# Performance work log

Hardware: AMD Instinct MI355X
Metric: run time of the kernel (lower is better)

The kernel has to match this reference:

```python
import jax, jax.numpy as jnp
from jax import lax
import numpy as np

BN_EPS = 1e-3  # ultralytics BatchNorm2d default eps

def setup_inputs() -> dict:
    key = jax.random.key(0)
    ks = jax.random.split(key, 6)
    B, C, H, W = 16, 64, 160, 160
    E, R = 4, 16  # experts, reduced router dim = C // reduction
    return {
        "x": jax.random.normal(ks[0], (B, C, H, W), jnp.float32),
        "fc1_w": jax.random.normal(ks[1], (R, C), jnp.float32) * 0.1,
        "fc2_w": jax.random.normal(ks[2], (E, R), jnp.float32) * 0.1,
        "fc2_b": jax.random.normal(ks[3], (E,), jnp.float32) * 0.1,
        "conv_w": jax.random.normal(ks[4], (E, C, C, 3, 3), jnp.float32) * 0.05,
        "bn_gamma": jnp.ones((E, C), jnp.float32),
        "bn_beta": jnp.zeros((E, C), jnp.float32),
        "bn_mean": jax.random.normal(ks[5], (E, C), jnp.float32) * 0.1,
        "bn_var": jnp.ones((E, C), jnp.float32),
    }

def reference(x, fc1_w, fc2_w, fc2_b, conv_w, bn_gamma, bn_beta, bn_mean, bn_var):
    # Router: global avg pool -> fc1 -> relu -> fc2 -> softmax over experts
    g = jnp.mean(x, axis=(2, 3))                       # [B, C]
    h = jax.nn.relu(g @ fc1_w.T)                       # [B, R]
    w = jax.nn.softmax(h @ fc2_w.T + fc2_b, axis=1)    # [B, E]

    def expert(kernel, gamma, beta, mean, var):
        # Conv2d(bias=False, pad=k//2) + BatchNorm2d (eval) + SiLU
        y = lax.conv_general_dilated(
            x, kernel, window_strides=(1, 1), padding="SAME",
            dimension_numbers=("NCHW", "OIHW", "NCHW"))
        scale = (gamma * lax.rsqrt(var + BN_EPS))[None, :, None, None]
        shift = (beta - mean * gamma * lax.rsqrt(var + BN_EPS))[None, :, None, None]
        return jax.nn.silu(y * scale + shift)          # [B, Co, H, W]

    outs = jax.vmap(expert)(conv_w, bn_gamma, bn_beta, bn_mean, bn_var)  # [E, B, Co, H, W]
    return jnp.einsum("ebchw,be->bchw", outs, w)
```

## Files before the change

kernel.cpp:

```cpp
#include <hip/hip_runtime.h>
#include <hip/hip_bf16.h>

typedef unsigned short u16;
typedef unsigned int   u32;
typedef __attribute__((ext_vector_type(8))) short s16x8;
typedef __attribute__((ext_vector_type(16))) float f32x16;

#define BN_EPS 1e-3f
#define NB 16
#define NC 64
#define NH 160
#define NW 160
#define HP 162
#define WPD 162

#define OFF_XT 0UL
#define SZ_XT  (16UL*162*162*64*2)
#define OFF_WT (OFF_XT + SZ_XT)
#define SZ_WT  (4UL*64*9*64*2)
#define OFF_SH (OFF_WT + SZ_WT)
#define OFF_G  (OFF_SH + 1024UL)
#define OFF_WE (OFF_G + 4096UL)
#define OFF_GP (OFF_WE + 256UL)

#define XSTRIDE 342
#define XLS_BYTES (8 * XSTRIDE * 16)
#define WLS_BYTES (2304 * 16)
#define SHLS_BYTES 1024
#define SMEM_TOTAL (XLS_BYTES + WLS_BYTES + SHLS_BYTES)

__device__ __forceinline__ u16 f2bf(float f) {
    u32 u = __builtin_bit_cast(u32, f);
    u += 0x7fffu + ((u >> 16) & 1u);
    return (u16)(u >> 16);
}

__global__ void prep_w(const float* __restrict__ cw, u16* __restrict__ wt,
                       const float* __restrict__ gamma, const float* __restrict__ beta,
                       const float* __restrict__ mean, const float* __restrict__ var,
                       float* __restrict__ shift) {
    int idx = blockIdx.x * 256 + threadIdx.x;
    if (idx < 4 * 2 * 9 * 4 * 64 * 8) {
        int cin = idx & 7;
        int t = idx >> 3;
        int co = t & 63; t >>= 6;
        int cio = t & 3; t >>= 2;
        int pos = t % 9; t /= 9;
        int ch = t & 1;
        int e = t >> 1;
        int tsp = (pos % 3) * 3 + (pos / 3);
        int ci = ch * 32 + cio * 8 + cin;
        int ec = e * 64 + co;
        float sc = gamma[ec] * rsqrtf(var[ec] + BN_EPS);
        wt[idx] = f2bf(cw[(((long)ec) * 64 + ci) * 9 + tsp] * sc);
    }
    if (idx < 256) {
        float sc = gamma[idx] * rsqrtf(var[idx] + BN_EPS);
        shift[idx] = beta[idx] - mean[idx] * sc;
    }
}

__global__ void prep_x(const float* __restrict__ x, u16* __restrict__ xt,
                       float* __restrict__ gpart) {
    __shared__ float tile[64][33];
    int blk = blockIdx.x;
    int t = threadIdx.x;
    if (blk >= 12800) {
        int bb = blk - 12800;
        int hp = bb % 162, b = bb / 162;
        u32* row = (u32*)xt + (((long)b * 162 + hp) * 162) * 32;
        if (hp == 0 || hp == 161) {
            for (int i = t; i < 162 * 32; i += 256) row[i] = 0u;
        } else if (t < 64) {
            int p = (t >> 5) ? 161 : 0;
            row[p * 32 + (t & 31)] = 0u;
        }
        return;
    }
    int wt5 = blk % 5;
    int tmp = blk / 5;
    int h = tmp % 160, b = tmp / 160;
    int w0 = wt5 * 32;
    int w = t & 31, c0 = t >> 5;
#pragma unroll
    for (int i = 0; i < 8; ++i) {
        int c = c0 + 8 * i;
        tile[c][w] = x[(((long)b * 64 + c) * 160 + h) * 160 + w0 + w];
    }
    __syncthreads();
    if (t < 64) {
        float s = 0.f;
#pragma unroll
        for (int wi = 0; wi < 32; ++wi) s += tile[t][wi];
        gpart[((long)(b * 64 + t)) * 800 + h * 5 + wt5] = s;
    }
    u32* xt32 = (u32*)xt;
    long base = ((((long)b * 162 + h + 1) * 162) + (w0 + 1)) * 32;
#pragma unroll
    for (int j = 0; j < 4; ++j) {
        int idx = t + 256 * j;
        int p = idx >> 5, cp = idx & 31;
        float v0 = tile[2 * cp][p], v1 = tile[2 * cp + 1][p];
        xt32[base + p * 32 + cp] = (u32)f2bf(v0) | ((u32)f2bf(v1) << 16);
    }
}

__global__ void g_reduce(const float* __restrict__ gpart, float* __restrict__ g) {
    int id = blockIdx.x;
    int t = threadIdx.x;
    float s = 0.f;
    for (int i = t; i < 800; i += 256) s += gpart[(long)id * 800 + i];
#pragma unroll
    for (int off = 32; off > 0; off >>= 1) s += __shfl_down(s, off, 64);
    __shared__ float red[4];
    if ((t & 63) == 0) red[t >> 6] = s;
    __syncthreads();
    if (t == 0) g[id] = (red[0] + red[1] + red[2] + red[3]) * (1.f / 25600.f);
}

__global__ void router(const float* __restrict__ g, const float* __restrict__ fc1w,
                       const float* __restrict__ fc2w, const float* __restrict__ fc2b,
                       float* __restrict__ wexp) {
    __shared__ float gL[16][64];
    __shared__ float h1[16][16];
    __shared__ float z[16][4];
    int t = threadIdx.x;
    for (int i = t; i < 1024; i += 256) gL[i >> 6][i & 63] = g[i];
    __syncthreads();
    {
        int b = t >> 4, r = t & 15;
        float s = 0.f;
#pragma unroll
        for (int c = 0; c < 64; ++c) s += gL[b][c] * fc1w[r * 64 + c];
        h1[b][r] = fmaxf(s, 0.f);
    }
    __syncthreads();
    if (t < 64) {
        int b = t >> 2, e = t & 3;
        float s = fc2b[e];
#pragma unroll
        for (int r = 0; r < 16; ++r) s += h1[b][r] * fc2w[e * 16 + r];
        z[b][e] = s;
    }
    __syncthreads();
    if (t < 16) {
        int b = t;
        float m = fmaxf(fmaxf(z[b][0], z[b][1]), fmaxf(z[b][2], z[b][3]));
        float e0 = __expf(z[b][0] - m), e1 = __expf(z[b][1] - m);
        float e2 = __expf(z[b][2] - m), e3 = __expf(z[b][3] - m);
        float inv = 1.f / (e0 + e1 + e2 + e3);
        wexp[b * 4 + 0] = e0 * inv; wexp[b * 4 + 1] = e1 * inv;
        wexp[b * 4 + 2] = e2 * inv; wexp[b * 4 + 3] = e3 * inv;
    }
}

__global__ __launch_bounds__(256, 2) void conv_main(
    const u16* __restrict__ xt, const u16* __restrict__ wt,
    const float* __restrict__ shift,
    const float* __restrict__ wexp, float* __restrict__ out) {
    extern __shared__ char smem[];
    u16* xls = (u16*)smem;
    u16* wls = (u16*)(smem + XLS_BYTES);
    float* shls = (float*)(smem + XLS_BYTES + WLS_BYTES);

    const int o = blockIdx.x;
    const int blk = (o & 7) * 200 + (o >> 3);
    const int wt5 = blk % 5;
    const int tmp = blk / 5;
    const int ht = tmp % 20;
    const int b = tmp / 20;
    const int h0 = ht * 8, w0 = wt5 * 32;
    const int tid = threadIdx.x;
    const int lane = tid & 63;
    const int wv = tid >> 6;
    const int l31 = lane & 31, kh = lane >> 5;
    const int r0 = 2 * wv;

    {
#pragma unroll
        for (int r = 0; r < 9; ++r) {
            int oo = r * 256 + tid;
            __builtin_amdgcn_global_load_lds(
                (const __attribute__((address_space(1))) void*)(wt + oo * 8),
                (__attribute__((address_space(3))) void*)(wls + oo * 8),
                16, 0, 0);
        }
    }
    const float we0 = wexp[(b << 2) + 0];
    const float we1 = wexp[(b << 2) + 1];
    const float we2 = wexp[(b << 2) + 2];
    const float we3 = wexp[(b << 2) + 3];
    shls[tid] = shift[tid];
    {
        const u16* xb = xt + (long)b * HP * WPD * 64;
        for (int c = tid; c < 2720; c += 256) {
            int P = c >> 3, cg = c & 7;
            int y = P / 34, px = P - y * 34;
            const u16* src = xb + (((long)(h0 + y) * WPD) + (w0 + px)) * 64 + cg * 8;
            s16x8 v = *(const s16x8*)src;
            *(s16x8*)(&xls[(cg * XSTRIDE + P) << 3]) = v;
        }
    }

    const int oA2 = (kh * 64 + l31) << 3;
    const int oBk0 = ((kh * XSTRIDE) + r0 * 34 + l31) << 3;
    const int oBk1 = oBk0 + ((2 * XSTRIDE) << 3);

    f32x16 acc00 = (f32x16)(0.f), acc01 = (f32x16)(0.f);
    f32x16 acc10 = (f32x16)(0.f), acc11 = (f32x16)(0.f);
    f32x16 oac00 = (f32x16)(0.f), oac01 = (f32x16)(0.f);
    f32x16 oac10 = (f32x16)(0.f), oac11 = (f32x16)(0.f);

    auto epi = [&](int E) {
        const float we = (E == 0) ? we0 : (E == 1) ? we1 : (E == 2) ? we2 : we3;
        const float* shE = shls + (E << 6);
#pragma unroll
        for (int j = 0; j < 16; ++j) {
            const int cob = (j & 3) + 8 * (j >> 2) + 4 * kh;
            {
                float sh = shE[cob];
                float y0 = acc00[j] + sh;
                float y1 = acc01[j] + sh;
                oac00[j] += we * (y0 * __builtin_amdgcn_rcpf(1.f + __expf(-y0)));
                oac01[j] += we * (y1 * __builtin_amdgcn_rcpf(1.f + __expf(-y1)));
            }
            {
                float sh = shE[cob + 32];
                float y0 = acc10[j] + sh;
                float y1 = acc11[j] + sh;
                oac10[j] += we * (y0 * __builtin_amdgcn_rcpf(1.f + __expf(-y0)));
                oac11[j] += we * (y1 * __builtin_amdgcn_rcpf(1.f + __expf(-y1)));
            }
        }
        acc00 = (f32x16)(0.f); acc01 = (f32x16)(0.f);
        acc10 = (f32x16)(0.f); acc11 = (f32x16)(0.f);
    };

#pragma unroll 1
    for (int s = 0; s < 8; ++s) {
        const int ch = s & 1;
        const int chU = (ch * 4 * XSTRIDE) << 3;
        const int b0U = oBk0 + chU;
        const int b1U = oBk1 + chU;

        auto dx_group = [&](int g, int pos0) {
            const int gU = g << 3;
            s16x8 B00 = *(const s16x8*)(&xls[b0U + gU]);
            s16x8 B01 = *(const s16x8*)(&xls[b1U + gU]);
            s16x8 B10 = *(const s16x8*)(&xls[b0U + gU + (34 << 3)]);
            s16x8 B11 = *(const s16x8*)(&xls[b1U + gU + (34 << 3)]);
            s16x8 B20 = *(const s16x8*)(&xls[b0U + gU + (68 << 3)]);
            s16x8 B21 = *(const s16x8*)(&xls[b1U + gU + (68 << 3)]);
            s16x8 B30 = *(const s16x8*)(&xls[b0U + gU + (102 << 3)]);
            s16x8 B31 = *(const s16x8*)(&xls[b1U + gU + (102 << 3)]);
            __builtin_amdgcn_s_setprio(1);
#pragma unroll
            for (int dy = 0; dy < 3; ++dy) {
                const int atU = oA2 + (pos0 + dy) * 2048;
                s16x8 a00 = *(const s16x8*)(&wls[atU]);
                s16x8 a10 = *(const s16x8*)(&wls[atU + 256]);
                s16x8 a01 = *(const s16x8*)(&wls[atU + 1024]);
                s16x8 a11 = *(const s16x8*)(&wls[atU + 1280]);
                s16x8 bn00 = (dy == 0) ? B00 : (dy == 1) ? B10 : B20;
                s16x8 bn01 = (dy == 0) ? B01 : (dy == 1) ? B11 : B21;
                s16x8 bn10 = (dy == 0) ? B10 : (dy == 1) ? B20 : B30;
                s16x8 bn11 = (dy == 0) ? B11 : (dy == 1) ? B21 : B31;
                acc00 = __builtin_amdgcn_mfma_f32_32x32x16_bf16(a00, bn00, acc00, 0, 0, 0);
                acc10 = __builtin_amdgcn_mfma_f32_32x32x16_bf16(a10, bn00, acc10, 0, 0, 0);
                acc01 = __builtin_amdgcn_mfma_f32_32x32x16_bf16(a00, bn10, acc01, 0, 0, 0);
                acc11 = __builtin_amdgcn_mfma_f32_32x32x16_bf16(a10, bn10, acc11, 0, 0, 0);
                acc00 = __builtin_amdgcn_mfma_f32_32x32x16_bf16(a01, bn01, acc00, 0, 0, 0);
                acc10 = __builtin_amdgcn_mfma_f32_32x32x16_bf16(a11, bn01, acc10, 0, 0, 0);
                acc01 = __builtin_amdgcn_mfma_f32_32x32x16_bf16(a01, bn11, acc01, 0, 0, 0);
                acc11 = __builtin_amdgcn_mfma_f32_32x32x16_bf16(a11, bn11, acc11, 0, 0, 0);
            }
            __builtin_amdgcn_s_setprio(0);
        };

        if (s == 0) __builtin_amdgcn_s_waitcnt(0x070);
        else        __builtin_amdgcn_s_waitcnt(0xF73);
        __builtin_amdgcn_s_barrier();
        __builtin_amdgcn_sched_barrier(0);
        dx_group(0, 0);
        dx_group(1, 3);

        __builtin_amdgcn_s_waitcnt(0xF70);
        __builtin_amdgcn_s_barrier();
        __builtin_amdgcn_sched_barrier(0);
        if (s < 7) {
            const u16* wsrc = wt + ((long)(s + 1)) * 2304 * 8;
#pragma unroll
            for (int r = 0; r < 6; ++r) {
                int oo = r * 256 + tid;
                __builtin_amdgcn_global_load_lds(
                    (const __attribute__((address_space(1))) void*)(wsrc + oo * 8),
                    (__attribute__((address_space(3))) void*)(wls + oo * 8),
                    16, 0, 0);
            }
        }
        dx_group(2, 6);
        if (ch == 1) epi(s >> 1);

        __builtin_amdgcn_s_barrier();
        __builtin_amdgcn_sched_barrier(0);
        if (s < 7) {
            const u16* wsrc = wt + ((long)(s + 1)) * 2304 * 8;
#pragma unroll
            for (int r = 6; r < 9; ++r) {
                int oo = r * 256 + tid;
                __builtin_amdgcn_global_load_lds(
                    (const __attribute__((address_space(1))) void*)(wsrc + oo * 8),
                    (__attribute__((address_space(3))) void*)(wls + oo * 8),
                    16, 0, 0);
            }
        }
    }

    const int yy = h0 + r0;
#pragma unroll
    for (int j = 0; j < 16; ++j) {
        const int cob = (j & 3) + 8 * (j >> 2) + 4 * kh;
        out[(((long)(b * 64 + cob)) * 160 + yy) * 160 + w0 + l31] = oac00[j];
        out[(((long)(b * 64 + cob)) * 160 + yy + 1) * 160 + w0 + l31] = oac01[j];
        out[(((long)(b * 64 + cob + 32)) * 160 + yy) * 160 + w0 + l31] = oac10[j];
        out[(((long)(b * 64 + cob + 32)) * 160 + yy + 1) * 160 + w0 + l31] = oac11[j];
    }
}

extern "C" void kernel_launch(void* const* d_in, const int* in_sizes, int n_in,
                              void* d_out, int out_size, void* d_ws, size_t ws_size,
                              hipStream_t stream) {
    const float* x = (const float*)d_in[0];
    const float* fc1w = (const float*)d_in[1];
    const float* fc2w = (const float*)d_in[2];
    const float* fc2b = (const float*)d_in[3];
    const float* convw = (const float*)d_in[4];
    const float* gamma = (const float*)d_in[5];
    const float* beta = (const float*)d_in[6];
    const float* mean = (const float*)d_in[7];
    const float* var = (const float*)d_in[8];
    float* out = (float*)d_out;
    char* ws = (char*)d_ws;
    u16* xt = (u16*)(ws + OFF_XT);
    u16* wtb = (u16*)(ws + OFF_WT);
    float* shift = (float*)(ws + OFF_SH);
    float* g = (float*)(ws + OFF_G);
    float* wexp = (float*)(ws + OFF_WE);
    float* gpart = (float*)(ws + OFF_GP);

    hipFuncSetAttribute((const void*)conv_main,
                        hipFuncAttributeMaxDynamicSharedMemorySize, SMEM_TOTAL);

    prep_w<<<576, 256, 0, stream>>>(convw, wtb, gamma, beta, mean, var, shift);
    prep_x<<<15392, 256, 0, stream>>>(x, xt, gpart);
    g_reduce<<<1024, 256, 0, stream>>>(gpart, g);
    router<<<1, 256, 0, stream>>>(g, fc1w, fc2w, fc2b, wexp);
    conv_main<<<1600, 256, SMEM_TOTAL, stream>>>(xt, wtb, shift, wexp, out);
}
```

Measured before the change: 178.4 us.

## Make conv kernel persistent with per-XCD atomic tile queues

Replaces the 1600-block launch with 512 persistent blocks that take tiles from eight per-XCD atomic counters, stealing from other queues when their own runs out. Weight prefetch now wraps around so the next tile's first expert chunk is already loading, which removes per-block launch and ramp-up cost and the tail imbalance. The cost is an extra memset, an atomic and a barrier per tile, and the x-tile load is no longer overlapped with block startup. There is also a possible hazard from the x LDS overwrite racing with the previous tile's reads.

```diff
diff --git a/kernel.cpp b/kernel.cpp
--- a/kernel.cpp
+++ b/kernel.cpp
@@ -21,13 +21,14 @@
 #define OFF_SH (OFF_WT + SZ_WT)
 #define OFF_G  (OFF_SH + 1024UL)
 #define OFF_WE (OFF_G + 4096UL)
-#define OFF_GP (OFF_WE + 256UL)
+#define OFF_CT (OFF_WE + 256UL)
+#define OFF_GP (OFF_CT + 256UL)
 
 #define XSTRIDE 342
 #define XLS_BYTES (8 * XSTRIDE * 16)
 #define WLS_BYTES (2304 * 16)
 #define SHLS_BYTES 1024
-#define SMEM_TOTAL (XLS_BYTES + WLS_BYTES + SHLS_BYTES)
+#define SMEM_TOTAL (XLS_BYTES + WLS_BYTES + SHLS_BYTES + 16)
 
 __device__ __forceinline__ u16 f2bf(float f) {
     u32 u = __builtin_bit_cast(u32, f);
@@ -157,24 +158,20 @@
 __global__ __launch_bounds__(256, 2) void conv_main(
     const u16* __restrict__ xt, const u16* __restrict__ wt,
     const float* __restrict__ shift,
-    const float* __restrict__ wexp, float* __restrict__ out) {
+    const float* __restrict__ wexp, float* __restrict__ out,
+    u32* __restrict__ ctrs) {
     extern __shared__ char smem[];
     u16* xls = (u16*)smem;
     u16* wls = (u16*)(smem + XLS_BYTES);
     float* shls = (float*)(smem + XLS_BYTES + WLS_BYTES);
-
-    const int o = blockIdx.x;
-    const int blk = (o & 7) * 200 + (o >> 3);
-    const int wt5 = blk % 5;
-    const int tmp = blk / 5;
-    const int ht = tmp % 20;
-    const int b = tmp / 20;
-    const int h0 = ht * 8, w0 = wt5 * 32;
+    int* stl = (int*)(smem + XLS_BYTES + WLS_BYTES + SHLS_BYTES);
+
     const int tid = threadIdx.x;
     const int lane = tid & 63;
     const int wv = tid >> 6;
     const int l31 = lane & 31, kh = lane >> 5;
     const int r0 = 2 * wv;
+    const int xb8 = blockIdx.x & 7;
 
     {
 #pragma unroll
@@ -186,145 +183,170 @@
                 16, 0, 0);
         }
     }
-    const float we0 = wexp[(b << 2) + 0];
-    const float we1 = wexp[(b << 2) + 1];
-    const float we2 = wexp[(b << 2) + 2];
-    const float we3 = wexp[(b << 2) + 3];
     shls[tid] = shift[tid];
-    {
-        const u16* xb = xt + (long)b * HP * WPD * 64;
-        for (int c = tid; c < 2720; c += 256) {
-            int P = c >> 3, cg = c & 7;
-            int y = P / 34, px = P - y * 34;
-            const u16* src = xb + (((long)(h0 + y) * WPD) + (w0 + px)) * 64 + cg * 8;
-            s16x8 v = *(const s16x8*)src;
-            *(s16x8*)(&xls[(cg * XSTRIDE + P) << 3]) = v;
-        }
-    }
 
     const int oA2 = (kh * 64 + l31) << 3;
     const int oBk0 = ((kh * XSTRIDE) + r0 * 34 + l31) << 3;
     const int oBk1 = oBk0 + ((2 * XSTRIDE) << 3);
 
-    f32x16 acc00 = (f32x16)(0.f), acc01 = (f32x16)(0.f);
-    f32x16 acc10 = (f32x16)(0.f), acc11 = (f32x16)(0.f);
-    f32x16 oac00 = (f32x16)(0.f), oac01 = (f32x16)(0.f);
-    f32x16 oac10 = (f32x16)(0.f), oac11 = (f32x16)(0.f);
-
-    auto epi = [&](int E) {
-        const float we = (E == 0) ? we0 : (E == 1) ? we1 : (E == 2) ? we2 : we3;
-        const float* shE = shls + (E << 6);
+    for (;;) {
+        if (tid == 0) {
+            int got = -1;
+            for (int d = 0; d < 8; ++d) {
+                int xx = (xb8 + d) & 7;
+                u32 tl = atomicAdd(&ctrs[xx], 1u);
+                if (tl < 200u) { got = xx * 200 + (int)tl; break; }
+            }
+            *stl = got;
+        }
+        __syncthreads();
+        const int blk = *stl;
+        if (blk < 0) break;
+
+        const int wt5 = blk % 5;
+        const int tmp = blk / 5;
+        const int ht = tmp % 20;
+        const int b = tmp / 20;
+        const int h0 = ht * 8, w0 = wt5 * 32;
+
+        const float we0 = wexp[(b << 2) + 0];
+        const float we1 = wexp[(b << 2) + 1];
+        const float we2 = wexp[(b << 2) + 2];
+        const float we3 = wexp[(b << 2) + 3];
+
+        {
+            const u16* xb = xt + (long)b * HP * WPD * 64;
+            for (int c = tid; c < 2720; c += 256) {
+                int P = c >> 3, cg = c & 7;
+                int y = P / 34, px = P - y * 34;
+                const u16* src = xb + (((long)(h0 + y) * WPD) + (w0 + px)) * 64 + cg * 8;
+                s16x8 v = *(const s16x8*)src;
+                *(s16x8*)(&xls[(cg * XSTRIDE + P) << 3]) = v;
+            }
+        }
+
+        f32x16 acc00 = (f32x16)(0.f), acc01 = (f32x16)(0.f);
+        f32x16 acc10 = (f32x16)(0.f), acc11 = (f32x16)(0.f);
+        f32x16 oac00 = (f32x16)(0.f), oac01 = (f32x16)(0.f);
+        f32x16 oac10 = (f32x16)(0.f), oac11 = (f32x16)(0.f);
+
+        auto epi = [&](int E) {
+            const float we = (E == 0) ? we0 : (E == 1) ? we1 : (E == 2) ? we2 : we3;
+            const float* shE = shls + (E << 6);
+#pragma unroll
+            for (int j = 0; j < 16; ++j) {
+                const int cob = (j & 3) + 8 * (j >> 2) + 4 * kh;
+                {
+                    float sh = shE[cob];
+                    float y0 = acc00[j] + sh;
+                    float y1 = acc01[j] + sh;
+                    oac00[j] += we * (y0 * __builtin_amdgcn_rcpf(1.f + __expf(-y0)));
+                    oac01[j] += we * (y1 * __builtin_amdgcn_rcpf(1.f + __expf(-y1)));
+                }
+                {
+                    float sh = shE[cob + 32];
+                    float y0 = acc10[j] + sh;
+                    float y1 = acc11[j] + sh;
+                    oac10[j] += we * (y0 * __builtin_amdgcn_rcpf(1.f + __expf(-y0)));
+                    oac11[j] += we * (y1 * __builtin_amdgcn_rcpf(1.f + __expf(-y1)));
+                }
+            }
+            acc00 = (f32x16)(0.f); acc01 = (f32x16)(0.f);
+            acc10 = (f32x16)(0.f); acc11 = (f32x16)(0.f);
+        };
+
+#pragma unroll 1
+        for (int s = 0; s < 8; ++s) {
+            const int ch = s & 1;
+            const int chU = (ch * 4 * XSTRIDE) << 3;
+            const int b0U = oBk0 + chU;
+            const int b1U = oBk1 + chU;
+            const int sn = (s + 1) & 7;
+
+            auto dx_group = [&](int g, int pos0) {
+                const int gU = g << 3;
+                s16x8 B00 = *(const s16x8*)(&xls[b0U + gU]);
+                s16x8 B01 = *(const s16x8*)(&xls[b1U + gU]);
+                s16x8 B10 = *(const s16x8*)(&xls[b0U + gU + (34 << 3)]);
+                s16x8 B11 = *(const s16x8*)(&xls[b1U + gU + (34 << 3)]);
+                s16x8 B20 = *(const s16x8*)(&xls[b0U + gU + (68 << 3)]);
+                s16x8 B21 = *(const s16x8*)(&xls[b1U + gU + (68 << 3)]);
+                s16x8 B30 = *(const s16x8*)(&xls[b0U + gU + (102 << 3)]);
+                s16x8 B31 = *(const s16x8*)(&xls[b1U + gU + (102 << 3)]);
+                __builtin_amdgcn_s_setprio(1);
+#pragma unroll
+                for (int dy = 0; dy < 3; ++dy) {
+                    const int atU = oA2 + (pos0 + dy) * 2048;
+                    s16x8 a00 = *(const s16x8*)(&wls[atU]);
+                    s16x8 a10 = *(const s16x8*)(&wls[atU + 256]);
+                    s16x8 a01 = *(const s16x8*)(&wls[atU + 1024]);
+                    s16x8 a11 = *(const s16x8*)(&wls[atU + 1280]);
+                    s16x8 bn00 = (dy == 0) ? B00 : (dy == 1) ? B10 : B20;
+                    s16x8 bn01 = (dy == 0) ? B01 : (dy == 1) ? B11 : B21;
+                    s16x8 bn10 = (dy == 0) ? B10 : (dy == 1) ? B20 : B30;
+                    s16x8 bn11 = (dy == 0) ? B11 : (dy == 1) ? B21 : B31;
+                    acc00 = __builtin_amdgcn_mfma_f32_32x32x16_bf16(a00, bn00, acc00, 0, 0, 0);
+                    acc10 = __builtin_amdgcn_mfma_f32_32x32x16_bf16(a10, bn00, acc10, 0, 0, 0);
+                    acc01 = __builtin_amdgcn_mfma_f32_32x32x16_bf16(a00, bn10, acc01, 0, 0, 0);
+                    acc11 = __builtin_amdgcn_mfma_f32_32x32x16_bf16(a10, bn10, acc11, 0, 0, 0);
+                    acc00 = __builtin_amdgcn_mfma_f32_32x32x16_bf16(a01, bn01, acc00, 0, 0, 0);
+                    acc10 = __builtin_amdgcn_mfma_f32_32x32x16_bf16(a11, bn01, acc10, 0, 0, 0);
+                    acc01 = __builtin_amdgcn_mfma_f32_32x32x16_bf16(a01, bn11, acc01, 0, 0, 0);
+                    acc11 = __builtin_amdgcn_mfma_f32_32x32x16_bf16(a11, bn11, acc11, 0, 0, 0);
+                }
+                __builtin_amdgcn_s_setprio(0);
+            };
+
+            if (s == 0) __builtin_amdgcn_s_waitcnt(0x070);
+            else        __builtin_amdgcn_s_waitcnt(0xF73);
+            __builtin_amdgcn_s_barrier();
+            __builtin_amdgcn_sched_barrier(0);
+            dx_group(0, 0);
+            dx_group(1, 3);
+
+            __builtin_amdgcn_s_waitcnt(0xF70);
+            __builtin_amdgcn_s_barrier();
+            __builtin_amdgcn_sched_barrier(0);
+            {
+                const u16* wsrc = wt + ((long)sn) * 2304 * 8;
+#pragma unroll
+                for (int r = 0; r < 6; ++r) {
+                    int oo = r * 256 + tid;
+                    __builtin_amdgcn_global_load_lds(
+                        (const __attribute__((address_space(1))) void*)(wsrc + oo * 8),
+                        (__attribute__((address_space(3))) void*)(wls + oo * 8),
+                        16, 0, 0);
+                }
+            }
+            dx_group(2, 6);
+            if (ch == 1) epi(s >> 1);
+
+            __builtin_amdgcn_s_barrier();
+            __builtin_amdgcn_sched_barrier(0);
+            {
+                const u16* wsrc = wt + ((long)sn) * 2304 * 8;
+#pragma unroll
+                for (int r = 6; r < 9; ++r) {
+                    int oo = r * 256 + tid;
+                    __builtin_amdgcn_global_load_lds(
+                        (const __attribute__((address_space(1))) void*)(wsrc + oo * 8),
+                        (__attribute__((address_space(3))) void*)(wls + oo * 8),
+                        16, 0, 0);
+                }
+            }
+        }
+
+        const int yy = h0 + r0;
 #pragma unroll
         for (int j = 0; j < 16; ++j) {
             const int cob = (j & 3) + 8 * (j >> 2) + 4 * kh;
-            {
-                float sh = shE[cob];
-                float y0 = acc00[j] + sh;
-                float y1 = acc01[j] + sh;
-                oac00[j] += we * (y0 * __builtin_amdgcn_rcpf(1.f + __expf(-y0)));
-                oac01[j] += we * (y1 * __builtin_amdgcn_rcpf(1.f + __expf(-y1)));
-            }
-            {
-                float sh = shE[cob + 32];
-                float y0 = acc10[j] + sh;
-                float y1 = acc11[j] + sh;
-                oac10[j] += we * (y0 * __builtin_amdgcn_rcpf(1.f + __expf(-y0)));
-                oac11[j] += we * (y1 * __builtin_amdgcn_rcpf(1.f + __expf(-y1)));
-            }
-        }
-        acc00 = (f32x16)(0.f); acc01 = (f32x16)(0.f);
-        acc10 = (f32x16)(0.f); acc11 = (f32x16)(0.f);
-    };
-
-#pragma unroll 1
-    for (int s = 0; s < 8; ++s) {
-        const int ch = s & 1;
-        const int chU = (ch * 4 * XSTRIDE) << 3;
-        const int b0U = oBk0 + chU;
-        const int b1U = oBk1 + chU;
-
-        auto dx_group = [&](int g, int pos0) {
-            const int gU = g << 3;
-            s16x8 B00 = *(const s16x8*)(&xls[b0U + gU]);
-            s16x8 B01 = *(const s16x8*)(&xls[b1U + gU]);
-            s16x8 B10 = *(const s16x8*)(&xls[b0U + gU + (34 << 3)]);
-            s16x8 B11 = *(const s16x8*)(&xls[b1U + gU + (34 << 3)]);
-            s16x8 B20 = *(const s16x8*)(&xls[b0U + gU + (68 << 3)]);
-            s16x8 B21 = *(const s16x8*)(&xls[b1U + gU + (68 << 3)]);
-            s16x8 B30 = *(const s16x8*)(&xls[b0U + gU + (102 << 3)]);
-            s16x8 B31 = *(const s16x8*)(&xls[b1U + gU + (102 << 3)]);
-            __builtin_amdgcn_s_setprio(1);
-#pragma unroll
-            for (int dy = 0; dy < 3; ++dy) {
-                const int atU = oA2 + (pos0 + dy) * 2048;
-                s16x8 a00 = *(const s16x8*)(&wls[atU]);
-                s16x8 a10 = *(const s16x8*)(&wls[atU + 256]);
-                s16x8 a01 = *(const s16x8*)(&wls[atU + 1024]);
-                s16x8 a11 = *(const s16x8*)(&wls[atU + 1280]);
-                s16x8 bn00 = (dy == 0) ? B00 : (dy == 1) ? B10 : B20;
-                s16x8 bn01 = (dy == 0) ? B01 : (dy == 1) ? B11 : B21;
-                s16x8 bn10 = (dy == 0) ? B10 : (dy == 1) ? B20 : B30;
-                s16x8 bn11 = (dy == 0) ? B11 : (dy == 1) ? B21 : B31;
-                acc00 = __builtin_amdgcn_mfma_f32_32x32x16_bf16(a00, bn00, acc00, 0, 0, 0);
-                acc10 = __builtin_amdgcn_mfma_f32_32x32x16_bf16(a10, bn00, acc10, 0, 0, 0);
-                acc01 = __builtin_amdgcn_mfma_f32_32x32x16_bf16(a00, bn10, acc01, 0, 0, 0);
-                acc11 = __builtin_amdgcn_mfma_f32_32x32x16_bf16(a10, bn10, acc11, 0, 0, 0);
-                acc00 = __builtin_amdgcn_mfma_f32_32x32x16_bf16(a01, bn01, acc00, 0, 0, 0);
-                acc10 = __builtin_amdgcn_mfma_f32_32x32x16_bf16(a11, bn01, acc10, 0, 0, 0);
-                acc01 = __builtin_amdgcn_mfma_f32_32x32x16_bf16(a01, bn11, acc01, 0, 0, 0);
-                acc11 = __builtin_amdgcn_mfma_f32_32x32x16_bf16(a11, bn11, acc11, 0, 0, 0);
-            }
-            __builtin_amdgcn_s_setprio(0);
-        };
-
-        if (s == 0) __builtin_amdgcn_s_waitcnt(0x070);
-        else        __builtin_amdgcn_s_waitcnt(0xF73);
-        __builtin_amdgcn_s_barrier();
-        __builtin_amdgcn_sched_barrier(0);
-        dx_group(0, 0);
-        dx_group(1, 3);
-
-        __builtin_amdgcn_s_waitcnt(0xF70);
-        __builtin_amdgcn_s_barrier();
-        __builtin_amdgcn_sched_barrier(0);
-        if (s < 7) {
-            const u16* wsrc = wt + ((long)(s + 1)) * 2304 * 8;
-#pragma unroll
-            for (int r = 0; r < 6; ++r) {
-                int oo = r * 256 + tid;
-                __builtin_amdgcn_global_load_lds(
-                    (const __attribute__((address_space(1))) void*)(wsrc + oo * 8),
-                    (__attribute__((address_space(3))) void*)(wls + oo * 8),
-                    16, 0, 0);
-            }
-        }
-        dx_group(2, 6);
-        if (ch == 1) epi(s >> 1);
-
-        __builtin_amdgcn_s_barrier();
-        __builtin_amdgcn_sched_barrier(0);
-        if (s < 7) {
-            const u16* wsrc = wt + ((long)(s + 1)) * 2304 * 8;
-#pragma unroll
-            for (int r = 6; r < 9; ++r) {
-                int oo = r * 256 + tid;
-                __builtin_amdgcn_global_load_lds(
-                    (const __attribute__((address_space(1))) void*)(wsrc + oo * 8),
-                    (__attribute__((address_space(3))) void*)(wls + oo * 8),
-                    16, 0, 0);
-            }
-        }
-    }
-
-    const int yy = h0 + r0;
-#pragma unroll
-    for (int j = 0; j < 16; ++j) {
-        const int cob = (j & 3) + 8 * (j >> 2) + 4 * kh;
-        out[(((long)(b * 64 + cob)) * 160 + yy) * 160 + w0 + l31] = oac00[j];
-        out[(((long)(b * 64 + cob)) * 160 + yy + 1) * 160 + w0 + l31] = oac01[j];
-        out[(((long)(b * 64 + cob + 32)) * 160 + yy) * 160 + w0 + l31] = oac10[j];
-        out[(((long)(b * 64 + cob + 32)) * 160 + yy + 1) * 160 + w0 + l31] = oac11[j];
-    }
+            out[(((long)(b * 64 + cob)) * 160 + yy) * 160 + w0 + l31] = oac00[j];
+            out[(((long)(b * 64 + cob)) * 160 + yy + 1) * 160 + w0 + l31] = oac01[j];
+            out[(((long)(b * 64 + cob + 32)) * 160 + yy) * 160 + w0 + l31] = oac10[j];
+            out[(((long)(b * 64 + cob + 32)) * 160 + yy + 1) * 160 + w0 + l31] = oac11[j];
+        }
+    }
+    __builtin_amdgcn_s_waitcnt(0xF70);
 }
 
 extern "C" void kernel_launch(void* const* d_in, const int* in_sizes, int n_in,
@@ -346,14 +368,16 @@
     float* shift = (float*)(ws + OFF_SH);
     float* g = (float*)(ws + OFF_G);
     float* wexp = (float*)(ws + OFF_WE);
+    u32* ctrs = (u32*)(ws + OFF_CT);
     float* gpart = (float*)(ws + OFF_GP);
 
     hipFuncSetAttribute((const void*)conv_main,
                         hipFuncAttributeMaxDynamicSharedMemorySize, SMEM_TOTAL);
 
+    hipMemsetAsync(ctrs, 0, 32, stream);
     prep_w<<<576, 256, 0, stream>>>(convw, wtb, gamma, beta, mean, var, shift);
     prep_x<<<15392, 256, 0, stream>>>(x, xt, gpart);
     g_reduce<<<1024, 256, 0, stream>>>(gpart, g);
     router<<<1, 256, 0, stream>>>(g, fc1w, fc2w, fc2b, wexp);
-    conv_main<<<1600, 256, SMEM_TOTAL, stream>>>(xt, wtb, shift, wexp, out);
-}
+    conv_main<<<512, 256, SMEM_TOTAL, stream>>>(xt, wtb, shift, wexp, out, ctrs);
+}
```

Result: slower. 241.7 us (+35.5%).

## Double-buffer weight slices in LDS with half-size K stages

Applied to the files above, without the earlier changes.

Splits each expert/channel-half weight stage into two 16-channel sub-stages, giving 16 smaller stages in place of 8. The LDS weight area becomes two 1152-entry buffers used in ping-pong fashion, and prep_w is relaid out to match. The next stage's weights are prefetched into the other buffer by 192 threads right after one barrier per stage, replacing the split mid-stage loads and the extra barriers. Fewer barriers and better overlap of loads with MFMA work come at the cost of fewer MFMAs per barrier and twice as many loop iterations.

```diff
diff --git a/kernel.cpp b/kernel.cpp
--- a/kernel.cpp
+++ b/kernel.cpp
@@ -25,7 +25,7 @@
 
 #define XSTRIDE 342
 #define XLS_BYTES (8 * XSTRIDE * 16)
-#define WLS_BYTES (2304 * 16)
+#define WLS_BYTES (2 * 1152 * 16)
 #define SHLS_BYTES 1024
 #define SMEM_TOTAL (XLS_BYTES + WLS_BYTES + SHLS_BYTES)
 
@@ -40,16 +40,16 @@
                        const float* __restrict__ mean, const float* __restrict__ var,
                        float* __restrict__ shift) {
     int idx = blockIdx.x * 256 + threadIdx.x;
-    if (idx < 4 * 2 * 9 * 4 * 64 * 8) {
+    if (idx < 16 * 9 * 2 * 64 * 8) {
         int cin = idx & 7;
-        int t = idx >> 3;
-        int co = t & 63; t >>= 6;
-        int cio = t & 3; t >>= 2;
-        int pos = t % 9; t /= 9;
-        int ch = t & 1;
-        int e = t >> 1;
+        int o = idx >> 3;
+        int co = o & 63; o >>= 6;
+        int kh = o & 1;  o >>= 1;
+        int pos = o % 9; o /= 9;
+        int s = o;
+        int ks = s & 1, ch = (s >> 1) & 1, e = s >> 2;
         int tsp = (pos % 3) * 3 + (pos / 3);
-        int ci = ch * 32 + cio * 8 + cin;
+        int ci = ch * 32 + ks * 16 + kh * 8 + cin;
         int ec = e * 64 + co;
         float sc = gamma[ec] * rsqrtf(var[ec] + BN_EPS);
         wt[idx] = f2bf(cw[(((long)ec) * 64 + ci) * 9 + tsp] * sc);
@@ -176,10 +176,10 @@
     const int l31 = lane & 31, kh = lane >> 5;
     const int r0 = 2 * wv;
 
-    {
-#pragma unroll
-        for (int r = 0; r < 9; ++r) {
-            int oo = r * 256 + tid;
+    if (tid < 192) {
+#pragma unroll
+        for (int r = 0; r < 6; ++r) {
+            int oo = r * 192 + tid;
             __builtin_amdgcn_global_load_lds(
                 (const __attribute__((address_space(1))) void*)(wt + oo * 8),
                 (__attribute__((address_space(3))) void*)(wls + oo * 8),
@@ -201,10 +201,6 @@
             *(s16x8*)(&xls[(cg * XSTRIDE + P) << 3]) = v;
         }
     }
-
-    const int oA2 = (kh * 64 + l31) << 3;
-    const int oBk0 = ((kh * XSTRIDE) + r0 * 34 + l31) << 3;
-    const int oBk1 = oBk0 + ((2 * XSTRIDE) << 3);
 
     f32x16 acc00 = (f32x16)(0.f), acc01 = (f32x16)(0.f);
     f32x16 acc10 = (f32x16)(0.f), acc11 = (f32x16)(0.f);
@@ -237,83 +233,57 @@
     };
 
 #pragma unroll 1
-    for (int s = 0; s < 8; ++s) {
-        const int ch = s & 1;
-        const int chU = (ch * 4 * XSTRIDE) << 3;
-        const int b0U = oBk0 + chU;
-        const int b1U = oBk1 + chU;
+    for (int s = 0; s < 16; ++s) {
+        const int ks = s & 1, ch = (s >> 1) & 1;
+        const int wbU = (s & 1) * 9216;
+
+        if (s == 0) __builtin_amdgcn_s_waitcnt(0x070);
+        else        __builtin_amdgcn_s_waitcnt(0xF70);
+        __builtin_amdgcn_s_barrier();
+        __builtin_amdgcn_sched_barrier(0);
+
+        if (s < 15 && tid < 192) {
+            const u16* wsrc = wt + (long)(s + 1) * 9216;
+            const int dbU = ((s + 1) & 1) * 9216;
+#pragma unroll
+            for (int r = 0; r < 6; ++r) {
+                int oo = r * 192 + tid;
+                __builtin_amdgcn_global_load_lds(
+                    (const __attribute__((address_space(1))) void*)(wsrc + oo * 8),
+                    (__attribute__((address_space(3))) void*)(wls + dbU + oo * 8),
+                    16, 0, 0);
+            }
+        }
+
+        const int bU = (((ch * 4 + ks * 2 + kh) * XSTRIDE) + r0 * 34 + l31) << 3;
 
         auto dx_group = [&](int g, int pos0) {
             const int gU = g << 3;
-            s16x8 B00 = *(const s16x8*)(&xls[b0U + gU]);
-            s16x8 B01 = *(const s16x8*)(&xls[b1U + gU]);
-            s16x8 B10 = *(const s16x8*)(&xls[b0U + gU + (34 << 3)]);
-            s16x8 B11 = *(const s16x8*)(&xls[b1U + gU + (34 << 3)]);
-            s16x8 B20 = *(const s16x8*)(&xls[b0U + gU + (68 << 3)]);
-            s16x8 B21 = *(const s16x8*)(&xls[b1U + gU + (68 << 3)]);
-            s16x8 B30 = *(const s16x8*)(&xls[b0U + gU + (102 << 3)]);
-            s16x8 B31 = *(const s16x8*)(&xls[b1U + gU + (102 << 3)]);
+            s16x8 B0 = *(const s16x8*)(&xls[bU + gU]);
+            s16x8 B1 = *(const s16x8*)(&xls[bU + gU + (34 << 3)]);
+            s16x8 B2 = *(const s16x8*)(&xls[bU + gU + (68 << 3)]);
+            s16x8 B3 = *(const s16x8*)(&xls[bU + gU + (102 << 3)]);
             __builtin_amdgcn_s_setprio(1);
 #pragma unroll
             for (int dy = 0; dy < 3; ++dy) {
-                const int atU = oA2 + (pos0 + dy) * 2048;
-                s16x8 a00 = *(const s16x8*)(&wls[atU]);
-                s16x8 a10 = *(const s16x8*)(&wls[atU + 256]);
-                s16x8 a01 = *(const s16x8*)(&wls[atU + 1024]);
-                s16x8 a11 = *(const s16x8*)(&wls[atU + 1280]);
-                s16x8 bn00 = (dy == 0) ? B00 : (dy == 1) ? B10 : B20;
-                s16x8 bn01 = (dy == 0) ? B01 : (dy == 1) ? B11 : B21;
-                s16x8 bn10 = (dy == 0) ? B10 : (dy == 1) ? B20 : B30;
-                s16x8 bn11 = (dy == 0) ? B11 : (dy == 1) ? B21 : B31;
-                acc00 = __builtin_amdgcn_mfma_f32_32x32x16_bf16(a00, bn00, acc00, 0, 0, 0);
-                acc10 = __builtin_amdgcn_mfma_f32_32x32x16_bf16(a10, bn00, acc10, 0, 0, 0);
-                acc01 = __builtin_amdgcn_mfma_f32_32x32x16_bf16(a00, bn10, acc01, 0, 0, 0);
-                acc11 = __builtin_amdgcn_mfma_f32_32x32x16_bf16(a10, bn10, acc11, 0, 0, 0);
-                acc00 = __builtin_amdgcn_mfma_f32_32x32x16_bf16(a01, bn01, acc00, 0, 0, 0);
-                acc10 = __builtin_amdgcn_mfma_f32_32x32x16_bf16(a11, bn01, acc10, 0, 0, 0);
-                acc01 = __builtin_amdgcn_mfma_f32_32x32x16_bf16(a01, bn11, acc01, 0, 0, 0);
-                acc11 = __builtin_amdgcn_mfma_f32_32x32x16_bf16(a11, bn11, acc11, 0, 0, 0);
+                const int atU = wbU + ((((pos0 + dy) * 2 + kh) * 64 + l31) << 3);
+                s16x8 a0 = *(const s16x8*)(&wls[atU]);
+                s16x8 a1 = *(const s16x8*)(&wls[atU + 256]);
+                s16x8 bn0 = (dy == 0) ? B0 : (dy == 1) ? B1 : B2;
+                s16x8 bn1 = (dy == 0) ? B1 : (dy == 1) ? B2 : B3;
+                acc00 = __builtin_amdgcn_mfma_f32_32x32x16_bf16(a0, bn0, acc00, 0, 0, 0);
+                acc10 = __builtin_amdgcn_mfma_f32_32x32x16_bf16(a1, bn0, acc10, 0, 0, 0);
+                acc01 = __builtin_amdgcn_mfma_f32_32x32x16_bf16(a0, bn1, acc01, 0, 0, 0);
+                acc11 = __builtin_amdgcn_mfma_f32_32x32x16_bf16(a1, bn1, acc11, 0, 0, 0);
             }
             __builtin_amdgcn_s_setprio(0);
         };
 
-        if (s == 0) __builtin_amdgcn_s_waitcnt(0x070);
-        else        __builtin_amdgcn_s_waitcnt(0xF73);
-        __builtin_amdgcn_s_barrier();
-        __builtin_amdgcn_sched_barrier(0);
         dx_group(0, 0);
         dx_group(1, 3);
-
-        __builtin_amdgcn_s_waitcnt(0xF70);
-        __builtin_amdgcn_s_barrier();
-        __builtin_amdgcn_sched_barrier(0);
-        if (s < 7) {
-            const u16* wsrc = wt + ((long)(s + 1)) * 2304 * 8;
-#pragma unroll
-            for (int r = 0; r < 6; ++r) {
-                int oo = r * 256 + tid;
-                __builtin_amdgcn_global_load_lds(
-                    (const __attribute__((address_space(1))) void*)(wsrc + oo * 8),
-                    (__attribute__((address_space(3))) void*)(wls + oo * 8),
-                    16, 0, 0);
-            }
-        }
         dx_group(2, 6);
-        if (ch == 1) epi(s >> 1);
-
-        __builtin_amdgcn_s_barrier();
-        __builtin_amdgcn_sched_barrier(0);
-        if (s < 7) {
-            const u16* wsrc = wt + ((long)(s + 1)) * 2304 * 8;
-#pragma unroll
-            for (int r = 6; r < 9; ++r) {
-                int oo = r * 256 + tid;
-                __builtin_amdgcn_global_load_lds(
-                    (const __attribute__((address_space(1))) void*)(wsrc + oo * 8),
-                    (__attribute__((address_space(3))) void*)(wls + oo * 8),
-                    16, 0, 0);
-            }
-        }
+
+        if ((s & 3) == 3) epi(s >> 2);
     }
 
     const int yy = h0 + r0;
```

After: 180.1 us. Within noise of the previous version (+1.0%).
